# Optimization experiments

Measured on AMD Instinct MI355X. Metric: run time of the kernel, lower is better.

## Reference

```python
import jax, jax.numpy as jnp
import numpy as np

# Coefficients of the 16 differentiable logic gates expressed over the basis
# [1, a, b, a*b]. Row i corresponds to gate i in the standard difflogic order:
# 0:0, 1:a&b, 2:a&~b, 3:a, 4:~a&b, 5:b, 6:xor, 7:or, 8:nor, 9:xnor,
# 10:~b, 11:b=>a, 12:~a, 13:a=>b, 14:nand, 15:1
GATE_COEFFS = np.array([
    [0, 0, 0, 0],
    [0, 0, 0, 1],
    [0, 1, 0, -1],
    [0, 1, 0, 0],
    [0, 0, 1, -1],
    [0, 0, 1, 0],
    [0, 1, 1, -2],
    [0, 1, 1, -1],
    [1, -1, -1, 1],
    [1, -1, -1, 2],
    [1, 0, -1, 0],
    [1, 0, -1, 1],
    [1, -1, 0, 0],
    [1, -1, 0, 1],
    [1, 0, 0, -1],
    [1, 0, 0, 0],
], dtype=np.float32)

IN_DIM = 8192
OUT_DIM = 8192
BATCH = 8192
TAU = 1.0


def setup_inputs() -> dict:
    key = jax.random.key(0)
    k1, k2, k3, k4 = jax.random.split(key, 4)
    x = jax.random.uniform(k1, (BATCH, IN_DIM), dtype=jnp.float32)
    weight = jax.random.normal(k2, (OUT_DIM, 16), dtype=jnp.float32)
    idx_a = jax.random.randint(k3, (OUT_DIM,), 0, IN_DIM, dtype=jnp.int64 if jax.config.jax_enable_x64 else jnp.int32)
    idx_b = jax.random.randint(k4, (OUT_DIM,), 0, IN_DIM, dtype=jnp.int64 if jax.config.jax_enable_x64 else jnp.int32)
    return {"x": x, "weight": weight, "idx_a": idx_a, "idx_b": idx_b}


def reference(x, weight, idx_a, idx_b):
    # Gather the two inputs of each neuron: [B, out_dim]
    a = x[:, idx_a]
    b = x[:, idx_b]
    # Soft gate mixture: softmax over 16 gates per neuron (training, 'soft')
    w = jax.nn.softmax(weight / TAU, axis=-1)  # [out_dim, 16]
    # Since every gate is affine in {1, a, b, ab}, collapse the 16-gate
    # weighted sum into per-neuron coefficients: c = w @ G  -> [out_dim, 4]
    c = w @ jnp.asarray(GATE_COEFFS)
    out = c[:, 0] + c[:, 1] * a + c[:, 2] * b + c[:, 3] * (a * b)
    return out
```

## Files before the change

### kernel.cpp

```cpp
#include <hip/hip_runtime.h>
#include <math.h>

#define IN_DIM  8192
#define OUT_DIM 8192
#define BATCH   8192
#define ROWS    16
#define T       1024

#define GLOAD_LDS16(g, l) __builtin_amdgcn_global_load_lds( \
    (const __attribute__((address_space(1))) void*)(g),     \
    (__attribute__((address_space(3))) void*)(l), 16, 0, 0)

__device__ __constant__ float GC0[16] = {0,0,0,0, 0,0,0,0, 1,1,1,1, 1,1,1,1};
__device__ __constant__ float GC1[16] = {0,0,1,1, 0,0,1,1, -1,-1,0,0, -1,-1,0,0};
__device__ __constant__ float GC2[16] = {0,0,0,0, 1,1,1,1, -1,-1,-1,-1, 0,0,0,0};
__device__ __constant__ float GC3[16] = {0,1,-1,0, -1,0,-2,-1, 1,2,0,1, 0,1,-1,0};

__global__ __launch_bounds__(256) void compute_c_kernel(
    const float* __restrict__ weight, float4* __restrict__ c)
{
    int row = blockIdx.x * 256 + threadIdx.x;
    if (row >= OUT_DIM) return;
    const float* wr = weight + (size_t)row * 16;
    float v[16];
    float m = -1e30f;
#pragma unroll
    for (int i = 0; i < 16; ++i) { v[i] = wr[i]; m = fmaxf(m, v[i]); }
    float s = 0.f;
#pragma unroll
    for (int i = 0; i < 16; ++i) { v[i] = __expf(v[i] - m); s += v[i]; }
    float inv = 1.0f / s;
    float c0 = 0.f, c1 = 0.f, c2 = 0.f, c3 = 0.f;
#pragma unroll
    for (int i = 0; i < 16; ++i) {
        c0 = fmaf(v[i], GC0[i], c0);
        c1 = fmaf(v[i], GC1[i], c1);
        c2 = fmaf(v[i], GC2[i], c2);
        c3 = fmaf(v[i], GC3[i], c3);
    }
    c[row] = make_float4(c0 * inv, c1 * inv, c2 * inv, c3 * inv);
}

__global__ __launch_bounds__(T, 8) void gate_main_kernel(
    const float* __restrict__ x,
    const float4* __restrict__ c,
    const int4* __restrict__ ia4,
    const int4* __restrict__ ib4,
    float4* __restrict__ out)
{
    __shared__ float buf[2][IN_DIM];
    const int tid  = threadIdx.x;
    const int wave = tid >> 6;
    const size_t r0 = (size_t)blockIdx.x * ROWS;

    const int q0 = tid, q1 = tid + T;
    unsigned pkA0, pkA1, pkA2, pkA3, pkB0, pkB1, pkB2, pkB3;
    {
        int4 ia = ia4[q0], ib = ib4[q0];
        pkA0 = (unsigned)(ia.x << 2) | ((unsigned)(ib.x << 2) << 16);
        pkA1 = (unsigned)(ia.y << 2) | ((unsigned)(ib.y << 2) << 16);
        pkA2 = (unsigned)(ia.z << 2) | ((unsigned)(ib.z << 2) << 16);
        pkA3 = (unsigned)(ia.w << 2) | ((unsigned)(ib.w << 2) << 16);
        ia = ia4[q1]; ib = ib4[q1];
        pkB0 = (unsigned)(ia.x << 2) | ((unsigned)(ib.x << 2) << 16);
        pkB1 = (unsigned)(ia.y << 2) | ((unsigned)(ib.y << 2) << 16);
        pkB2 = (unsigned)(ia.z << 2) | ((unsigned)(ib.z << 2) << 16);
        pkB3 = (unsigned)(ia.w << 2) | ((unsigned)(ib.w << 2) << 16);
    }
    const float4 cA0 = c[4*q0+0], cA1 = c[4*q0+1], cA2 = c[4*q0+2], cA3 = c[4*q0+3];
    const float4 cB0 = c[4*q1+0], cB1 = c[4*q1+1], cB2 = c[4*q1+2], cB3 = c[4*q1+3];

    {
        const float* src = x + r0 * IN_DIM;
        GLOAD_LDS16(src + (tid << 2),        &buf[0][wave << 8]);
        GLOAD_LDS16(src + 4096 + (tid << 2), &buf[0][4096 + (wave << 8)]);
    }
    asm volatile("s_waitcnt vmcnt(0)" ::: "memory");
    __builtin_amdgcn_s_barrier();

    for (int r = 0; r < ROWS; ++r) {
        const int cur = r & 1;

        if (r + 1 < ROWS) {
            const float* src = x + (r0 + r + 1) * IN_DIM;
            float* bn = buf[cur ^ 1];
            GLOAD_LDS16(src + (tid << 2),        bn + (wave << 8));
            GLOAD_LDS16(src + 4096 + (tid << 2), bn + 4096 + (wave << 8));
        }
        asm volatile("" ::: "memory");

        const char* xb = (const char*)buf[cur];
        float4* orow = out + (r0 + r) * (OUT_DIM / 4);
        {
            float a0 = *(const float*)(xb + (pkA0 & 0xffffu));
            float b0 = *(const float*)(xb + (pkA0 >> 16));
            float a1 = *(const float*)(xb + (pkA1 & 0xffffu));
            float b1 = *(const float*)(xb + (pkA1 >> 16));
            float a2 = *(const float*)(xb + (pkA2 & 0xffffu));
            float b2 = *(const float*)(xb + (pkA2 >> 16));
            float a3 = *(const float*)(xb + (pkA3 & 0xffffu));
            float b3 = *(const float*)(xb + (pkA3 >> 16));
            float4 o;
            o.x = fmaf(a0, fmaf(b0, cA0.w, cA0.y), fmaf(b0, cA0.z, cA0.x));
            o.y = fmaf(a1, fmaf(b1, cA1.w, cA1.y), fmaf(b1, cA1.z, cA1.x));
            o.z = fmaf(a2, fmaf(b2, cA2.w, cA2.y), fmaf(b2, cA2.z, cA2.x));
            o.w = fmaf(a3, fmaf(b3, cA3.w, cA3.y), fmaf(b3, cA3.z, cA3.x));
            orow[q0] = o;
        }
        {
            float a0 = *(const float*)(xb + (pkB0 & 0xffffu));
            float b0 = *(const float*)(xb + (pkB0 >> 16));
            float a1 = *(const float*)(xb + (pkB1 & 0xffffu));
            float b1 = *(const float*)(xb + (pkB1 >> 16));
            float a2 = *(const float*)(xb + (pkB2 & 0xffffu));
            float b2 = *(const float*)(xb + (pkB2 >> 16));
            float a3 = *(const float*)(xb + (pkB3 & 0xffffu));
            float b3 = *(const float*)(xb + (pkB3 >> 16));
            float4 o;
            o.x = fmaf(a0, fmaf(b0, cB0.w, cB0.y), fmaf(b0, cB0.z, cB0.x));
            o.y = fmaf(a1, fmaf(b1, cB1.w, cB1.y), fmaf(b1, cB1.z, cB1.x));
            o.z = fmaf(a2, fmaf(b2, cB2.w, cB2.y), fmaf(b2, cB2.z, cB2.x));
            o.w = fmaf(a3, fmaf(b3, cB3.w, cB3.y), fmaf(b3, cB3.z, cB3.x));
            orow[q1] = o;
        }

        if (r + 1 < ROWS) {
            asm volatile("s_waitcnt vmcnt(2)" ::: "memory");
            __builtin_amdgcn_s_barrier();
        }
    }
}

extern "C" void kernel_launch(void* const* d_in, const int* in_sizes, int n_in,
                              void* d_out, int out_size, void* d_ws, size_t ws_size,
                              hipStream_t stream) {
    const float* x      = (const float*)d_in[0];
    const float* weight = (const float*)d_in[1];
    const int*   idx_a  = (const int*)d_in[2];
    const int*   idx_b  = (const int*)d_in[3];
    float* out = (float*)d_out;

    float4* c = (float4*)d_ws;

    compute_c_kernel<<<OUT_DIM / 256, 256, 0, stream>>>(weight, c);
    gate_main_kernel<<<BATCH / ROWS, T, 0, stream>>>(
        x, c, (const int4*)idx_a, (const int4*)idx_b, (float4*)out);
}
```

Measured before the change: 443.1 us.

## Fuse softmax coefficient computation into main gate kernel and drop max subtraction

Removes the separate coefficient kernel and has every block of the main kernel recompute the softmax-collapsed gate coefficients for its neurons directly from the weights. The first row prefetch into LDS is issued before this work so the exp math overlaps the load. The max subtraction is dropped, which saves ops but can overflow for large weights. Every one of the 512 blocks now redoes 16 exps per neuron for 8 neurons per thread and reads 64 floats of weight instead of 4, in exchange for one fewer launch and no workspace round trip.

```diff
diff --git a/kernel.cpp b/kernel.cpp
--- a/kernel.cpp
+++ b/kernel.cpp
@@ -11,39 +11,33 @@
     (const __attribute__((address_space(1))) void*)(g),     \
     (__attribute__((address_space(3))) void*)(l), 16, 0, 0)
 
-__device__ __constant__ float GC0[16] = {0,0,0,0, 0,0,0,0, 1,1,1,1, 1,1,1,1};
-__device__ __constant__ float GC1[16] = {0,0,1,1, 0,0,1,1, -1,-1,0,0, -1,-1,0,0};
-__device__ __constant__ float GC2[16] = {0,0,0,0, 1,1,1,1, -1,-1,-1,-1, 0,0,0,0};
-__device__ __constant__ float GC3[16] = {0,1,-1,0, -1,0,-2,-1, 1,2,0,1, 0,1,-1,0};
 
-__global__ __launch_bounds__(256) void compute_c_kernel(
-    const float* __restrict__ weight, float4* __restrict__ c)
+__device__ __forceinline__ float4 softmax_gate(const float* wr)
 {
-    int row = blockIdx.x * 256 + threadIdx.x;
-    if (row >= OUT_DIM) return;
-    const float* wr = weight + (size_t)row * 16;
-    float v[16];
-    float m = -1e30f;
+    const float4* w4 = (const float4*)wr;
+    float e[16];
 #pragma unroll
-    for (int i = 0; i < 16; ++i) { v[i] = wr[i]; m = fmaxf(m, v[i]); }
+    for (int k = 0; k < 4; ++k) {
+        float4 w = w4[k];
+        e[4*k+0] = __expf(w.x);
+        e[4*k+1] = __expf(w.y);
+        e[4*k+2] = __expf(w.z);
+        e[4*k+3] = __expf(w.w);
+    }
     float s = 0.f;
 #pragma unroll
-    for (int i = 0; i < 16; ++i) { v[i] = __expf(v[i] - m); s += v[i]; }
+    for (int i = 0; i < 16; ++i) s += e[i];
+    float g0 = e[8]+e[9]+e[10]+e[11]+e[12]+e[13]+e[14]+e[15];
+    float g1 = e[2]+e[3]+e[6]+e[7] - e[8]-e[9]-e[12]-e[13];
+    float g2 = e[4]+e[5]+e[6]+e[7] - e[8]-e[9]-e[10]-e[11];
+    float g3 = e[1]-e[2]-e[4]-2.f*e[6]-e[7]+e[8]+2.f*e[9]+e[11]+e[13]-e[14];
     float inv = 1.0f / s;
-    float c0 = 0.f, c1 = 0.f, c2 = 0.f, c3 = 0.f;
-#pragma unroll
-    for (int i = 0; i < 16; ++i) {
-        c0 = fmaf(v[i], GC0[i], c0);
-        c1 = fmaf(v[i], GC1[i], c1);
-        c2 = fmaf(v[i], GC2[i], c2);
-        c3 = fmaf(v[i], GC3[i], c3);
-    }
-    c[row] = make_float4(c0 * inv, c1 * inv, c2 * inv, c3 * inv);
+    return make_float4(g0*inv, g1*inv, g2*inv, g3*inv);
 }
 
 __global__ __launch_bounds__(T, 8) void gate_main_kernel(
     const float* __restrict__ x,
-    const float4* __restrict__ c,
+    const float* __restrict__ weight,
     const int4* __restrict__ ia4,
     const int4* __restrict__ ib4,
     float4* __restrict__ out)
@@ -52,6 +46,12 @@
     const int tid  = threadIdx.x;
     const int wave = tid >> 6;
     const size_t r0 = (size_t)blockIdx.x * ROWS;
+
+    {
+        const float* src = x + r0 * IN_DIM;
+        GLOAD_LDS16(src + (tid << 2),        &buf[0][wave << 8]);
+        GLOAD_LDS16(src + 4096 + (tid << 2), &buf[0][4096 + (wave << 8)]);
+    }
 
     const int q0 = tid, q1 = tid + T;
     unsigned pkA0, pkA1, pkA2, pkA3, pkB0, pkB1, pkB2, pkB3;
@@ -67,14 +67,16 @@
         pkB2 = (unsigned)(ia.z << 2) | ((unsigned)(ib.z << 2) << 16);
         pkB3 = (unsigned)(ia.w << 2) | ((unsigned)(ib.w << 2) << 16);
     }
-    const float4 cA0 = c[4*q0+0], cA1 = c[4*q0+1], cA2 = c[4*q0+2], cA3 = c[4*q0+3];
-    const float4 cB0 = c[4*q1+0], cB1 = c[4*q1+1], cB2 = c[4*q1+2], cB3 = c[4*q1+3];
 
-    {
-        const float* src = x + r0 * IN_DIM;
-        GLOAD_LDS16(src + (tid << 2),        &buf[0][wave << 8]);
-        GLOAD_LDS16(src + 4096 + (tid << 2), &buf[0][4096 + (wave << 8)]);
-    }
+    const float4 cA0 = softmax_gate(weight + (size_t)(4*q0+0) * 16);
+    const float4 cA1 = softmax_gate(weight + (size_t)(4*q0+1) * 16);
+    const float4 cA2 = softmax_gate(weight + (size_t)(4*q0+2) * 16);
+    const float4 cA3 = softmax_gate(weight + (size_t)(4*q0+3) * 16);
+    const float4 cB0 = softmax_gate(weight + (size_t)(4*q1+0) * 16);
+    const float4 cB1 = softmax_gate(weight + (size_t)(4*q1+1) * 16);
+    const float4 cB2 = softmax_gate(weight + (size_t)(4*q1+2) * 16);
+    const float4 cB3 = softmax_gate(weight + (size_t)(4*q1+3) * 16);
+
     asm volatile("s_waitcnt vmcnt(0)" ::: "memory");
     __builtin_amdgcn_s_barrier();
 
@@ -140,9 +142,6 @@
     const int*   idx_b  = (const int*)d_in[3];
     float* out = (float*)d_out;
 
-    float4* c = (float4*)d_ws;
-
-    compute_c_kernel<<<OUT_DIM / 256, 256, 0, stream>>>(weight, c);
     gate_main_kernel<<<BATCH / ROWS, T, 0, stream>>>(
-        x, c, (const int4*)idx_a, (const int4*)idx_b, (float4*)out);
+        x, weight, (const int4*)idx_a, (const int4*)idx_b, (float4*)out);
 }
```

New measurement: 561.1 us. 1.27x slower.
